# Performance work log

Hardware: AMD Instinct MI355X
Metric: run time of the kernel (lower is better)

The kernel has to match this reference:

```python
import jax, jax.numpy as jnp
import numpy as np

B, S, H = 8, 2048, 256

def setup_inputs() -> dict:
    key = jax.random.key(0)
    ks = jax.random.split(key, 7)
    sc = 0.05
    return {
        "inputs": jax.random.normal(ks[0], (B, S, H), dtype=jnp.float32),
        "Wq": jax.random.normal(ks[1], (H, H), dtype=jnp.float32) * sc,
        "bq": jax.random.normal(ks[2], (H,), dtype=jnp.float32) * sc,
        "Wk": jax.random.normal(ks[3], (H, H), dtype=jnp.float32) * sc,
        "bk": jax.random.normal(ks[4], (H,), dtype=jnp.float32) * sc,
        "Wv": jax.random.normal(ks[5], (H, H), dtype=jnp.float32) * sc,
        "bv": jax.random.normal(ks[6], (H,), dtype=jnp.float32) * sc,
    }

def reference(inputs, Wq, bq, Wk, bk, Wv, bv):
    # nn.Linear: y = x @ W.T + b
    q = jnp.einsum("bsh,oh->bso", inputs, Wq) + bq
    k = jnp.einsum("bsh,oh->bso", inputs, Wk) + bk
    v = jnp.einsum("bsh,oh->bso", inputs, Wv) + bv
    hidden = q.shape[-1]
    # NOTE: original scales by sqrt(hidden^2) == hidden (not sqrt(hidden))
    scores = jnp.einsum("bqh,bkh->bqk", q, k) / jnp.float32(hidden)
    # NOTE: original applies softmax over dim=1 (the query axis), not the last axis
    weights = jax.nn.softmax(scores, axis=1)
    return jnp.einsum("bqk,bkh->bqh", weights, v)
```

## Files before the change

### kernel.cpp

```cpp
#include <hip/hip_runtime.h>
#include <hip/hip_bf16.h>

#define B_ 8
#define S_ 2048
#define H_ 256
#define BS_ (B_*S_)

typedef __attribute__((ext_vector_type(8))) short bf16x8;
typedef __attribute__((ext_vector_type(4))) short bf16x4;
typedef __attribute__((ext_vector_type(4))) float f32x4;

static __device__ inline short f2bf(float f) {
  union { float f; unsigned int u; } a; a.f = f;
  unsigned int u = a.u;
  unsigned int r = (u + 0x7fffu + ((u >> 16) & 1u)) >> 16;
  return (short)r;
}

static __device__ inline float bf2f(short s) {
  union { float f; unsigned int u; } a;
  a.u = ((unsigned int)(unsigned short)s) << 16;
  return a.f;
}

static __device__ inline f32x4 mfma16(bf16x8 a, bf16x8 b, f32x4 c) {
  return __builtin_amdgcn_mfma_f32_16x16x32_bf16(a, b, c, 0, 0, 0);
}

static __device__ inline void gl_lds16(const short* g, short* l) {
  __builtin_amdgcn_global_load_lds(
      (const __attribute__((address_space(1))) void*)g,
      (__attribute__((address_space(3))) void*)l, 16, 0, 0);
}

#define NW4 (H_ * H_ / 4)
#define NWTOT (3 * NW4)
#define NALLW (NWTOT + BS_ / 4)

__global__ __launch_bounds__(256) void cvt_bf16(
    const float* __restrict__ Wq, const float* __restrict__ Wk,
    const float* __restrict__ Wv,
    short* __restrict__ wqb, short* __restrict__ wkb, short* __restrict__ wvb,
    float* __restrict__ den)
{
  int stride = gridDim.x * blockDim.x;
  for (int i = blockIdx.x * blockDim.x + threadIdx.x; i < NALLW; i += stride) {
    if (i >= NWTOT) {
      float4 z = {0.f, 0.f, 0.f, 0.f};
      *(float4*)(den + (size_t)(i - NWTOT) * 4) = z;
      continue;
    }
    int w = i >> 14;
    int off = i & (NW4 - 1);
    const float* src = (w == 0) ? Wq : (w == 1) ? Wk : Wv;
    short* dst = (w == 0) ? wqb : (w == 1) ? wkb : wvb;
    float4 v = *(const float4*)(src + off * 4);
    bf16x4 p;
    p[0] = f2bf(v.x); p[1] = f2bf(v.y); p[2] = f2bf(v.z); p[3] = f2bf(v.w);
    *(bf16x4*)(dst + off * 4) = p;
  }
}

__global__ __launch_bounds__(256) void qkv_proj(
    const float* __restrict__ x,
    const short* __restrict__ Wq, const float* __restrict__ bq,
    const short* __restrict__ Wk, const float* __restrict__ bk,
    const short* __restrict__ Wv, const float* __restrict__ bv,
    short* __restrict__ Qo, short* __restrict__ Ko, short* __restrict__ VTo)
{
  const int tid  = threadIdx.x;
  const int wave = tid >> 6;
  const int lane = tid & 63;
  const int quad = lane >> 4;
  const int l16  = lane & 15;
  const int y    = blockIdx.y;

  const short* W    = (y == 0) ? Wq : (y == 1) ? Wk : Wv;
  const float* bias = (y == 0) ? bq : (y == 1) ? bk : bv;
  const int sblk = blockIdx.x * 64;

  __shared__ short wbufA[16 * 512];
  __shared__ short xbufA[4 * 512];
  __shared__ short wbufB[16 * 512];
  __shared__ short xbufB[4 * 512];

  f32x4 zero = {0.f, 0.f, 0.f, 0.f};
  f32x4 acc[4][4];
#pragma unroll
  for (int i = 0; i < 4; i++)
#pragma unroll
    for (int j = 0; j < 4; j++) acc[i][j] = zero;

#define QKV_XLOAD(fa, fb, ch)                                             \
  {                                                                       \
    const float* xg = x + (size_t)(sblk + wave * 16 + l16) * H_ + (ch) * 32 + quad * 8; \
    fa = *(const float4*)xg;                                              \
    fb = *(const float4*)(xg + 4);                                        \
  }

#define QKV_XWRITE(xb_, fa, fb)                                           \
  {                                                                       \
    bf16x8 p;                                                             \
    p[0] = f2bf(fa.x); p[1] = f2bf(fa.y); p[2] = f2bf(fa.z); p[3] = f2bf(fa.w); \
    p[4] = f2bf(fb.x); p[5] = f2bf(fb.y); p[6] = f2bf(fb.z); p[7] = f2bf(fb.w); \
    *(bf16x8*)((xb_) + wave * 512 + lane * 8) = p;                        \
  }

#define QKV_STAGE_W(wb, ch)                                               \
  {                                                                       \
    _Pragma("unroll")                                                     \
    for (int i = 0; i < 4; i++) {                                         \
      int r = wave * 4 + i;                                               \
      gl_lds16(W + (r * 16 + l16) * H_ + (ch) * 32 + quad * 8, (wb) + r * 512); \
    }                                                                     \
  }

#define QKV_MFMA(wb, xb_)                                                 \
  {                                                                       \
    bf16x8 af[4];                                                         \
    _Pragma("unroll")                                                     \
    for (int st = 0; st < 4; st++)                                        \
      af[st] = *(const bf16x8*)((xb_) + st * 512 + lane * 8);             \
    _Pragma("unroll")                                                     \
    for (int i = 0; i < 4; i++) {                                         \
      bf16x8 bb = *(const bf16x8*)((wb) + (wave * 4 + i) * 512 + lane * 8); \
      _Pragma("unroll")                                                   \
      for (int st = 0; st < 4; st++)                                      \
        acc[st][i] = mfma16(af[st], bb, acc[st][i]);                      \
    }                                                                     \
  }

  float4 xa0, xb0, xa1, xb1;
  QKV_XLOAD(xa0, xb0, 0);
  QKV_STAGE_W(wbufA, 0);
  QKV_XWRITE(xbufA, xa0, xb0);
#pragma unroll
  for (int i2 = 0; i2 < 4; i2++) {
    __syncthreads();
    QKV_XLOAD(xa1, xb1, 2 * i2 + 1);
    QKV_STAGE_W(wbufB, 2 * i2 + 1);
    QKV_MFMA(wbufA, xbufA);
    QKV_XWRITE(xbufB, xa1, xb1);
    __syncthreads();
    if (i2 < 3) {
      QKV_XLOAD(xa0, xb0, 2 * i2 + 2);
      QKV_STAGE_W(wbufA, 2 * i2 + 2);
    }
    QKV_MFMA(wbufB, xbufB);
    if (i2 < 3) QKV_XWRITE(xbufA, xa0, xb0);
  }
#undef QKV_XLOAD
#undef QKV_XWRITE
#undef QKV_STAGE_W
#undef QKV_MFMA

  if (y < 2) {
    short* dst = (y == 0) ? Qo : Ko;
#pragma unroll
    for (int i = 0; i < 4; i++) {
      int col = (wave * 4 + i) * 16 + l16;
      float bvl = bias[col];
#pragma unroll
      for (int st = 0; st < 4; st++) {
#pragma unroll
        for (int r = 0; r < 4; r++) {
          int row = sblk + st * 16 + quad * 4 + r;
          dst[row * H_ + col] = f2bf(acc[st][i][r] + bvl);
        }
      }
    }
  } else {
#pragma unroll
    for (int i = 0; i < 4; i++) {
      int col = (wave * 4 + i) * 16 + l16;
      float bvl = bias[col];
#pragma unroll
      for (int st = 0; st < 4; st++) {
        int row0  = sblk + st * 16 + quad * 4;
        int b_idx = row0 >> 11;
        int k0    = row0 & (S_ - 1);
        bf16x4 pk;
#pragma unroll
        for (int r = 0; r < 4; r++) pk[r] = f2bf(acc[st][i][r] + bvl);
        *(bf16x4*)(VTo + (size_t)b_idx * H_ * S_ + (size_t)col * S_ + k0) = pk;
      }
    }
  }
}

__global__ __launch_bounds__(256, 2) void scores(
    const short* __restrict__ Q, const short* __restrict__ K,
    short* __restrict__ Pf, float* __restrict__ den)
{
  const int tid  = threadIdx.x;
  const int wave = tid >> 6;
  const int lane = tid & 63;
  const int quad = lane >> 4;
  const int l16  = lane & 15;
  const int ktg = blockIdx.x & 3;
  const int qt  = (blockIdx.x >> 2) & 15;
  const int b   = blockIdx.x >> 6;

  const short* Qb = Q + b * S_ * H_;
  const short* Kb = K + b * S_ * H_;
  const int qcol0 = qt * 128;

  __shared__ short qbuf[64 * 512];

  bf16x8 kreg[2][2][8];
  {
    const short* kb = Kb + ((ktg * 4) * 128 + wave * 32 + l16) * H_ + quad * 8;
#pragma unroll
    for (int kf = 0; kf < 2; kf++)
#pragma unroll
      for (int ch = 0; ch < 8; ch++)
        kreg[0][kf][ch] = *(const bf16x8*)(kb + kf * 16 * H_ + ch * 32);
  }

#pragma unroll
  for (int i = 0; i < 16; i++) {
    int region = wave * 16 + i;
    int qf = region >> 3;
    int ch = region & 7;
    gl_lds16(Qb + (qcol0 + qf * 16 + l16) * H_ + ch * 32 + quad * 8,
             qbuf + region * 512);
  }
  __syncthreads();

  const int quadA = quad >> 1;
  const int j0    = (quad & 1) * 4;

#pragma unroll
  for (int t = 0; t < 4; t++) {
    if (t < 3) {
      const short* kb = Kb + ((ktg * 4 + t + 1) * 128 + wave * 32 + l16) * H_ + quad * 8;
#pragma unroll
      for (int kf = 0; kf < 2; kf++)
#pragma unroll
        for (int ch = 0; ch < 8; ch++)
          kreg[(t + 1) & 1][kf][ch] = *(const bf16x8*)(kb + kf * 16 * H_ + ch * 32);
    }

    f32x4 zero = {0.f, 0.f, 0.f, 0.f};
    f32x4 acc[2][8];
#pragma unroll
    for (int i = 0; i < 2; i++)
#pragma unroll
      for (int j = 0; j < 8; j++) acc[i][j] = zero;

#pragma unroll
    for (int ch = 0; ch < 8; ch++) {
#pragma unroll
      for (int qf = 0; qf < 8; qf++) {
        bf16x8 bq = *(const bf16x8*)(qbuf + (qf * 8 + ch) * 512 + lane * 8);
        acc[0][qf] = mfma16(kreg[t & 1][0][ch], bq, acc[0][qf]);
        acc[1][qf] = mfma16(kreg[t & 1][1][ch], bq, acc[1][qf]);
      }
    }

    const int kt    = ktg * 4 + t;
    const int krow0 = kt * 128 + wave * 32;
    const int kw    = krow0 >> 5;

    float rs[2][4] = {{0.f,0.f,0.f,0.f},{0.f,0.f,0.f,0.f}};
#pragma unroll
    for (int kf = 0; kf < 2; kf++) {
#pragma unroll
      for (int qf = 0; qf < 8; qf++) {
        bf16x4 pk;
#pragma unroll
        for (int r = 0; r < 4; r++) {
          float e = __expf(acc[kf][qf][r] * (1.0f / H_));
          rs[kf][r] += e;
          pk[r] = f2bf(e);
        }
        size_t tile = ((size_t)(b * 128 + qt * 8 + qf) << 6) + kw;
        *(bf16x4*)(Pf + (tile << 9) + ((2 * kf + quadA) * 16 + l16) * 8 + j0) = pk;
      }
    }

#pragma unroll
    for (int kf = 0; kf < 2; kf++) {
#pragma unroll
      for (int r = 0; r < 4; r++) {
        float v = rs[kf][r];
        v += __shfl_xor(v, 1, 64);
        v += __shfl_xor(v, 2, 64);
        v += __shfl_xor(v, 4, 64);
        v += __shfl_xor(v, 8, 64);
        if (l16 == 0)
          atomicAdd(&den[b * S_ + krow0 + kf * 16 + quad * 4 + r], v);
      }
    }
  }
}

__global__ __launch_bounds__(256) void vscale(
    short* __restrict__ VT, const float* __restrict__ den)
{
  int i = blockIdx.x * 256 + threadIdx.x;
  int b  = i >> 17;
  int k0 = (i & 511) << 2;
  float4 df = *(const float4*)(den + b * S_ + k0);
  bf16x4 v = *(bf16x4*)(VT + (size_t)i * 4);
  bf16x4 o;
  o[0] = f2bf(bf2f(v[0]) / df.x);
  o[1] = f2bf(bf2f(v[1]) / df.y);
  o[2] = f2bf(bf2f(v[2]) / df.z);
  o[3] = f2bf(bf2f(v[3]) / df.w);
  *(bf16x4*)(VT + (size_t)i * 4) = o;
}

__global__ __launch_bounds__(256) void pv(
    const short* __restrict__ Pf, const short* __restrict__ VTs,
    float* __restrict__ out)
{
  const int tid  = threadIdx.x;
  const int wave = tid >> 6;
  const int lane = tid & 63;
  const int quad = lane >> 4;
  const int l16  = lane & 15;
  const int bx = blockIdx.x;
  const int qt = bx >> 4;
  const int b  = (bx >> 1) & 7;
  const int hs = bx & 1;

  __shared__ short vbufA[32 * 512];
  __shared__ short vbufB[32 * 512];

  const int qt16 = qt * 4 + wave;
  const short* VTb = VTs + (size_t)b * H_ * S_ + (size_t)(hs * 128) * S_;
  const size_t tilebase = ((size_t)(b * 128 + qt16) * 64) << 9;

  f32x4 zero = {0.f, 0.f, 0.f, 0.f};
  f32x4 acc[8];
#pragma unroll
  for (int i = 0; i < 8; i++) acc[i] = zero;

  bf16x8 pregA[4], pregB[4];

#define PV_STAGE_V(vb, kc)                                                  \
  {                                                                         \
    _Pragma("unroll")                                                       \
    for (int i = 0; i < 8; i++) {                                           \
      int id = wave * 8 + i;                                                \
      int n  = id >> 2;                                                     \
      int kw = id & 3;                                                      \
      const short* g = VTb + (size_t)(n * 16 + l16) * S_ + (kc) + kw * 32 + quad * 8; \
      gl_lds16(g, (vb) + id * 512);                                         \
    }                                                                       \
  }

#define PV_LOAD_P(pr, kc)                                                   \
  {                                                                         \
    _Pragma("unroll")                                                       \
    for (int kwi = 0; kwi < 4; kwi++)                                       \
      pr[kwi] = *(const bf16x8*)(Pf + tilebase + (size_t)(((kc) >> 5) + kwi) * 512 + lane * 8); \
  }

#define PV_MFMA(vb, pr)                                                     \
  {                                                                         \
    _Pragma("unroll")                                                       \
    for (int kw = 0; kw < 4; kw++) {                                        \
      _Pragma("unroll")                                                     \
      for (int n = 0; n < 8; n++) {                                         \
        bf16x8 vvb = *(const bf16x8*)((vb) + (n * 4 + kw) * 512 + lane * 8); \
        acc[n] = mfma16(pr[kw], vvb, acc[n]);                               \
      }                                                                     \
    }                                                                       \
  }

  PV_STAGE_V(vbufA, 0);
  PV_LOAD_P(pregA, 0);
#pragma unroll
  for (int i2 = 0; i2 < 8; i2++) {
    __syncthreads();
    PV_STAGE_V(vbufB, (2 * i2 + 1) * 128);
    PV_LOAD_P(pregB, (2 * i2 + 1) * 128);
    PV_MFMA(vbufA, pregA);
    __syncthreads();
    if (i2 < 7) {
      PV_STAGE_V(vbufA, (2 * i2 + 2) * 128);
      PV_LOAD_P(pregA, (2 * i2 + 2) * 128);
    }
    PV_MFMA(vbufB, pregB);
  }
#undef PV_STAGE_V
#undef PV_LOAD_P
#undef PV_MFMA

  const int q0 = qt16 * 16;
#pragma unroll
  for (int n = 0; n < 8; n++) {
    int col = hs * 128 + n * 16 + l16;
#pragma unroll
    for (int r = 0; r < 4; r++) {
      int q = q0 + quad * 4 + r;
      out[((size_t)b * S_ + q) * H_ + col] = acc[n][r];
    }
  }
}

extern "C" void kernel_launch(void* const* d_in, const int* in_sizes, int n_in,
                              void* d_out, int out_size, void* d_ws, size_t ws_size,
                              hipStream_t stream) {
  const float* x  = (const float*)d_in[0];
  const float* Wq = (const float*)d_in[1];
  const float* bq = (const float*)d_in[2];
  const float* Wk = (const float*)d_in[3];
  const float* bk = (const float*)d_in[4];
  const float* Wv = (const float*)d_in[5];
  const float* bv = (const float*)d_in[6];

  short* xb  = (short*)d_ws;
  short* wqb = xb  + (size_t)BS_ * H_;
  short* wkb = wqb + H_ * H_;
  short* wvb = wkb + H_ * H_;
  short* Qs  = wvb + H_ * H_;
  short* Ks  = Qs  + (size_t)BS_ * H_;
  short* VT  = Ks  + (size_t)BS_ * H_;
  short* P   = VT  + (size_t)BS_ * H_;
  float* den = (float*)(P + (size_t)B_ * S_ * S_);
  float* outp = (float*)d_out;

  cvt_bf16<<<208, 256, 0, stream>>>(Wq, Wk, Wv, wqb, wkb, wvb, den);
  qkv_proj<<<dim3(BS_ / 64, 3), 256, 0, stream>>>(x, wqb, bq, wkb, bk, wvb, bv, Qs, Ks, VT);
  scores<<<512, 256, 0, stream>>>(Qs, Ks, P, den);
  vscale<<<4096, 256, 0, stream>>>(VT, den);
  pv<<<512, 256, 0, stream>>>(P, VT, outp);
}
```

Baseline: 187.5 us.

## Recompute scores in fused PV kernel instead of materializing P matrix

The scores kernel now only accumulates the per-key softmax denominators and no longer writes the bf16 probability matrix. A fused PV kernel recomputes QK^T per 128-key chunk, applies exp and a reciprocal of the denominator, stages P in LDS and multiplies by V directly. This removes the large P write/read round trip through global memory and the separate vscale pass. The cost is doing the QK^T product twice, running a grid of 256 blocks at launch bounds of 1, and using single-buffered LDS with no prefetch of K or V.

```diff
diff --git a/kernel.cpp b/kernel.cpp
--- a/kernel.cpp
+++ b/kernel.cpp
@@ -188,9 +188,9 @@
   }
 }
 
-__global__ __launch_bounds__(256, 2) void scores(
+__global__ __launch_bounds__(256, 2) void scores_den(
     const short* __restrict__ Q, const short* __restrict__ K,
-    short* __restrict__ Pf, float* __restrict__ den)
+    float* __restrict__ den)
 {
   const int tid  = threadIdx.x;
   const int wave = tid >> 6;
@@ -227,9 +227,6 @@
   }
   __syncthreads();
 
-  const int quadA = quad >> 1;
-  const int j0    = (quad & 1) * 4;
-
 #pragma unroll
   for (int t = 0; t < 4; t++) {
     if (t < 3) {
@@ -258,24 +255,16 @@
       }
     }
 
-    const int kt    = ktg * 4 + t;
-    const int krow0 = kt * 128 + wave * 32;
-    const int kw    = krow0 >> 5;
+    const int krow0 = (ktg * 4 + t) * 128 + wave * 32;
 
     float rs[2][4] = {{0.f,0.f,0.f,0.f},{0.f,0.f,0.f,0.f}};
 #pragma unroll
     for (int kf = 0; kf < 2; kf++) {
 #pragma unroll
       for (int qf = 0; qf < 8; qf++) {
-        bf16x4 pk;
-#pragma unroll
-        for (int r = 0; r < 4; r++) {
-          float e = __expf(acc[kf][qf][r] * (1.0f / H_));
-          rs[kf][r] += e;
-          pk[r] = f2bf(e);
-        }
-        size_t tile = ((size_t)(b * 128 + qt * 8 + qf) << 6) + kw;
-        *(bf16x4*)(Pf + (tile << 9) + ((2 * kf + quadA) * 16 + l16) * 8 + j0) = pk;
+#pragma unroll
+        for (int r = 0; r < 4; r++)
+          rs[kf][r] += __expf(acc[kf][qf][r] * (1.0f / H_));
       }
     }
 
@@ -295,24 +284,9 @@
   }
 }
 
-__global__ __launch_bounds__(256) void vscale(
-    short* __restrict__ VT, const float* __restrict__ den)
-{
-  int i = blockIdx.x * 256 + threadIdx.x;
-  int b  = i >> 17;
-  int k0 = (i & 511) << 2;
-  float4 df = *(const float4*)(den + b * S_ + k0);
-  bf16x4 v = *(bf16x4*)(VT + (size_t)i * 4);
-  bf16x4 o;
-  o[0] = f2bf(bf2f(v[0]) / df.x);
-  o[1] = f2bf(bf2f(v[1]) / df.y);
-  o[2] = f2bf(bf2f(v[2]) / df.z);
-  o[3] = f2bf(bf2f(v[3]) / df.w);
-  *(bf16x4*)(VT + (size_t)i * 4) = o;
-}
-
-__global__ __launch_bounds__(256) void pv(
-    const short* __restrict__ Pf, const short* __restrict__ VTs,
+__global__ __launch_bounds__(256, 1) void pv_fused(
+    const short* __restrict__ Q, const short* __restrict__ K,
+    const short* __restrict__ VTs, const float* __restrict__ den,
     float* __restrict__ out)
 {
   const int tid  = threadIdx.x;
@@ -325,78 +299,127 @@
   const int b  = (bx >> 1) & 7;
   const int hs = bx & 1;
 
-  __shared__ short vbufA[32 * 512];
-  __shared__ short vbufB[32 * 512];
-
-  const int qt16 = qt * 4 + wave;
+  const short* Qb  = Q + b * S_ * H_;
+  const short* Kb  = K + b * S_ * H_;
   const short* VTb = VTs + (size_t)b * H_ * S_ + (size_t)(hs * 128) * S_;
-  const size_t tilebase = ((size_t)(b * 128 + qt16) * 64) << 9;
+  const float* denb = den + b * S_;
+  const int qcol0 = qt * 128;
+
+  __shared__ short qbuf[64 * 512];
+  __shared__ short pbuf[32 * 512];
+  __shared__ short vbuf[32 * 512];
 
   f32x4 zero = {0.f, 0.f, 0.f, 0.f};
-  f32x4 acc[8];
-#pragma unroll
-  for (int i = 0; i < 8; i++) acc[i] = zero;
-
-  bf16x8 pregA[4], pregB[4];
-
-#define PV_STAGE_V(vb, kc)                                                  \
-  {                                                                         \
-    _Pragma("unroll")                                                       \
-    for (int i = 0; i < 8; i++) {                                           \
-      int id = wave * 8 + i;                                                \
-      int n  = id >> 2;                                                     \
-      int kw = id & 3;                                                      \
-      const short* g = VTb + (size_t)(n * 16 + l16) * S_ + (kc) + kw * 32 + quad * 8; \
-      gl_lds16(g, (vb) + id * 512);                                         \
-    }                                                                       \
-  }
-
-#define PV_LOAD_P(pr, kc)                                                   \
-  {                                                                         \
-    _Pragma("unroll")                                                       \
-    for (int kwi = 0; kwi < 4; kwi++)                                       \
-      pr[kwi] = *(const bf16x8*)(Pf + tilebase + (size_t)(((kc) >> 5) + kwi) * 512 + lane * 8); \
-  }
-
-#define PV_MFMA(vb, pr)                                                     \
-  {                                                                         \
-    _Pragma("unroll")                                                       \
-    for (int kw = 0; kw < 4; kw++) {                                        \
-      _Pragma("unroll")                                                     \
-      for (int n = 0; n < 8; n++) {                                         \
-        bf16x8 vvb = *(const bf16x8*)((vb) + (n * 4 + kw) * 512 + lane * 8); \
-        acc[n] = mfma16(pr[kw], vvb, acc[n]);                               \
-      }                                                                     \
-    }                                                                       \
-  }
-
-  PV_STAGE_V(vbufA, 0);
-  PV_LOAD_P(pregA, 0);
-#pragma unroll
-  for (int i2 = 0; i2 < 8; i2++) {
+  f32x4 accpv[2][8];
+#pragma unroll
+  for (int i = 0; i < 2; i++)
+#pragma unroll
+    for (int j = 0; j < 8; j++) accpv[i][j] = zero;
+
+#pragma unroll
+  for (int i = 0; i < 16; i++) {
+    int region = wave * 16 + i;
+    int qf = region >> 3;
+    int ch = region & 7;
+    gl_lds16(Qb + (qcol0 + qf * 16 + l16) * H_ + ch * 32 + quad * 8,
+             qbuf + region * 512);
+  }
+  __syncthreads();
+
+  const int quadA = quad >> 1;
+  const int j0    = (quad & 1) * 4;
+
+  for (int t = 0; t < 16; t++) {
+    const int kc = t * 128;
+
+    bf16x8 kreg[2][8];
+    {
+      const short* kb = Kb + (kc + wave * 32 + l16) * H_ + quad * 8;
+#pragma unroll
+      for (int kf = 0; kf < 2; kf++)
+#pragma unroll
+        for (int ch = 0; ch < 8; ch++)
+          kreg[kf][ch] = *(const bf16x8*)(kb + kf * 16 * H_ + ch * 32);
+    }
+    float4 dv0 = *(const float4*)(denb + kc + wave * 32 + quad * 4);
+    float4 dv1 = *(const float4*)(denb + kc + wave * 32 + 16 + quad * 4);
+
+#pragma unroll
+    for (int i = 0; i < 8; i++) {
+      int id = wave * 8 + i;
+      int n  = id >> 2;
+      int kw = id & 3;
+      gl_lds16(VTb + (size_t)(n * 16 + l16) * S_ + kc + kw * 32 + quad * 8,
+               vbuf + id * 512);
+    }
+
+#pragma unroll
+    for (int kf = 0; kf < 2; kf++) {
+      f32x4 a8[8];
+#pragma unroll
+      for (int j = 0; j < 8; j++) a8[j] = zero;
+#pragma unroll
+      for (int ch = 0; ch < 8; ch++) {
+#pragma unroll
+        for (int qf = 0; qf < 8; qf++) {
+          bf16x8 bq = *(const bf16x8*)(qbuf + (qf * 8 + ch) * 512 + lane * 8);
+          a8[qf] = mfma16(kreg[kf][ch], bq, a8[qf]);
+        }
+      }
+      float rd[4];
+      {
+        float dd[4];
+        if (kf == 0) { dd[0]=dv0.x; dd[1]=dv0.y; dd[2]=dv0.z; dd[3]=dv0.w; }
+        else         { dd[0]=dv1.x; dd[1]=dv1.y; dd[2]=dv1.z; dd[3]=dv1.w; }
+#pragma unroll
+        for (int r = 0; r < 4; r++) {
+          float rc = __builtin_amdgcn_rcpf(dd[r]);
+          rc = rc * (2.0f - dd[r] * rc);
+          rd[r] = rc;
+        }
+      }
+#pragma unroll
+      for (int qf = 0; qf < 8; qf++) {
+        bf16x4 pk;
+#pragma unroll
+        for (int r = 0; r < 4; r++)
+          pk[r] = f2bf(__expf(a8[qf][r] * (1.0f / H_)) * rd[r]);
+        *(bf16x4*)(pbuf + (qf * 4 + wave) * 512 +
+                   ((2 * kf + quadA) * 16 + l16) * 8 + j0) = pk;
+      }
+    }
     __syncthreads();
-    PV_STAGE_V(vbufB, (2 * i2 + 1) * 128);
-    PV_LOAD_P(pregB, (2 * i2 + 1) * 128);
-    PV_MFMA(vbufA, pregA);
+
+#pragma unroll
+    for (int qsub = 0; qsub < 2; qsub++) {
+      const int qidx = wave * 2 + qsub;
+      bf16x8 preg[4];
+#pragma unroll
+      for (int ks = 0; ks < 4; ks++)
+        preg[ks] = *(const bf16x8*)(pbuf + (qidx * 4 + ks) * 512 + lane * 8);
+#pragma unroll
+      for (int ks = 0; ks < 4; ks++) {
+#pragma unroll
+        for (int n = 0; n < 8; n++) {
+          bf16x8 vvb = *(const bf16x8*)(vbuf + (n * 4 + ks) * 512 + lane * 8);
+          accpv[qsub][n] = mfma16(preg[ks], vvb, accpv[qsub][n]);
+        }
+      }
+    }
     __syncthreads();
-    if (i2 < 7) {
-      PV_STAGE_V(vbufA, (2 * i2 + 2) * 128);
-      PV_LOAD_P(pregA, (2 * i2 + 2) * 128);
-    }
-    PV_MFMA(vbufB, pregB);
-  }
-#undef PV_STAGE_V
-#undef PV_LOAD_P
-#undef PV_MFMA
-
-  const int q0 = qt16 * 16;
-#pragma unroll
-  for (int n = 0; n < 8; n++) {
-    int col = hs * 128 + n * 16 + l16;
-#pragma unroll
-    for (int r = 0; r < 4; r++) {
-      int q = q0 + quad * 4 + r;
-      out[((size_t)b * S_ + q) * H_ + col] = acc[n][r];
+  }
+
+#pragma unroll
+  for (int qsub = 0; qsub < 2; qsub++) {
+    const int q0 = qt * 128 + (wave * 2 + qsub) * 16;
+#pragma unroll
+    for (int n = 0; n < 8; n++) {
+      int col = hs * 128 + n * 16 + l16;
+#pragma unroll
+      for (int r = 0; r < 4; r++) {
+        int q = q0 + quad * 4 + r;
+        out[((size_t)b * S_ + q) * H_ + col] = accpv[qsub][n][r];
+      }
     }
   }
 }
@@ -425,7 +448,6 @@
 
   cvt_bf16<<<208, 256, 0, stream>>>(Wq, Wk, Wv, wqb, wkb, wvb, den);
   qkv_proj<<<dim3(BS_ / 64, 3), 256, 0, stream>>>(x, wqb, bq, wkb, bk, wvb, bv, Qs, Ks, VT);
-  scores<<<512, 256, 0, stream>>>(Qs, Ks, P, den);
-  vscale<<<4096, 256, 0, stream>>>(VT, den);
-  pv<<<512, 256, 0, stream>>>(P, VT, outp);
-}
+  scores_den<<<512, 256, 0, stream>>>(Qs, Ks, den);
+  pv_fused<<<256, 256, 0, stream>>>(Qs, Ks, VT, den, outp);
+}
```

New measurement: 236.0 us. +25.9%, slower.

## Recompute normalized scores inside PV kernel instead of materializing P

Applied to the files above, without the earlier changes.

The scores kernel now only accumulates column denominators. A new fused PV kernel recomputes Q·K^T per 128-key chunk, applies exp and reciprocal of the denominator, stages P in shared memory, and multiplies by V. This removes the large bf16 P write/read and the separate V scaling pass, at the cost of computing QK^T twice (once per head half as well) and a less overlapped pipeline with extra barriers.

```diff
diff --git a/kernel.cpp b/kernel.cpp
--- a/kernel.cpp
+++ b/kernel.cpp
@@ -188,9 +188,9 @@
   }
 }
 
-__global__ __launch_bounds__(256, 2) void scores(
+__global__ __launch_bounds__(256, 2) void scores_den(
     const short* __restrict__ Q, const short* __restrict__ K,
-    short* __restrict__ Pf, float* __restrict__ den)
+    float* __restrict__ den)
 {
   const int tid  = threadIdx.x;
   const int wave = tid >> 6;
@@ -227,9 +227,6 @@
   }
   __syncthreads();
 
-  const int quadA = quad >> 1;
-  const int j0    = (quad & 1) * 4;
-
 #pragma unroll
   for (int t = 0; t < 4; t++) {
     if (t < 3) {
@@ -258,24 +255,16 @@
       }
     }
 
-    const int kt    = ktg * 4 + t;
-    const int krow0 = kt * 128 + wave * 32;
-    const int kw    = krow0 >> 5;
+    const int krow0 = (ktg * 4 + t) * 128 + wave * 32;
 
     float rs[2][4] = {{0.f,0.f,0.f,0.f},{0.f,0.f,0.f,0.f}};
 #pragma unroll
     for (int kf = 0; kf < 2; kf++) {
 #pragma unroll
       for (int qf = 0; qf < 8; qf++) {
-        bf16x4 pk;
-#pragma unroll
-        for (int r = 0; r < 4; r++) {
-          float e = __expf(acc[kf][qf][r] * (1.0f / H_));
-          rs[kf][r] += e;
-          pk[r] = f2bf(e);
-        }
-        size_t tile = ((size_t)(b * 128 + qt * 8 + qf) << 6) + kw;
-        *(bf16x4*)(Pf + (tile << 9) + ((2 * kf + quadA) * 16 + l16) * 8 + j0) = pk;
+#pragma unroll
+        for (int r = 0; r < 4; r++)
+          rs[kf][r] += __expf(acc[kf][qf][r] * (1.0f / H_));
       }
     }
 
@@ -295,24 +284,9 @@
   }
 }
 
-__global__ __launch_bounds__(256) void vscale(
-    short* __restrict__ VT, const float* __restrict__ den)
-{
-  int i = blockIdx.x * 256 + threadIdx.x;
-  int b  = i >> 17;
-  int k0 = (i & 511) << 2;
-  float4 df = *(const float4*)(den + b * S_ + k0);
-  bf16x4 v = *(bf16x4*)(VT + (size_t)i * 4);
-  bf16x4 o;
-  o[0] = f2bf(bf2f(v[0]) / df.x);
-  o[1] = f2bf(bf2f(v[1]) / df.y);
-  o[2] = f2bf(bf2f(v[2]) / df.z);
-  o[3] = f2bf(bf2f(v[3]) / df.w);
-  *(bf16x4*)(VT + (size_t)i * 4) = o;
-}
-
-__global__ __launch_bounds__(256) void pv(
-    const short* __restrict__ Pf, const short* __restrict__ VTs,
+__global__ __launch_bounds__(256, 2) void pv_fused(
+    const short* __restrict__ Q, const short* __restrict__ K,
+    const short* __restrict__ VTs, const float* __restrict__ den,
     float* __restrict__ out)
 {
   const int tid  = threadIdx.x;
@@ -325,78 +299,133 @@
   const int b  = (bx >> 1) & 7;
   const int hs = bx & 1;
 
-  __shared__ short vbufA[32 * 512];
-  __shared__ short vbufB[32 * 512];
-
-  const int qt16 = qt * 4 + wave;
+  const short* Qb  = Q + b * S_ * H_;
+  const short* Kb  = K + b * S_ * H_;
   const short* VTb = VTs + (size_t)b * H_ * S_ + (size_t)(hs * 128) * S_;
-  const size_t tilebase = ((size_t)(b * 128 + qt16) * 64) << 9;
+  const float* denb = den + b * S_;
+  const int qcol0 = qt * 64;
+
+  __shared__ short qbuf[32 * 512];
+  __shared__ short pbuf[16 * 512];
+  __shared__ short vbuf[32 * 512];
 
   f32x4 zero = {0.f, 0.f, 0.f, 0.f};
-  f32x4 acc[8];
-#pragma unroll
-  for (int i = 0; i < 8; i++) acc[i] = zero;
-
-  bf16x8 pregA[4], pregB[4];
-
-#define PV_STAGE_V(vb, kc)                                                  \
+  f32x4 accpv[8];
+#pragma unroll
+  for (int i = 0; i < 8; i++) accpv[i] = zero;
+
+#pragma unroll
+  for (int i = 0; i < 8; i++) {
+    int region = wave * 8 + i;
+    int qf = region >> 3;
+    int ch = region & 7;
+    gl_lds16(Qb + (qcol0 + qf * 16 + l16) * H_ + ch * 32 + quad * 8,
+             qbuf + region * 512);
+  }
+
+  bf16x8 kregA[2][8], kregB[2][8];
+  float4 dvA0, dvA1, dvB0, dvB1;
+  {
+    const short* kb = Kb + (wave * 32 + l16) * H_ + quad * 8;
+#pragma unroll
+    for (int kf = 0; kf < 2; kf++)
+#pragma unroll
+      for (int ch = 0; ch < 8; ch++)
+        kregA[kf][ch] = *(const bf16x8*)(kb + kf * 16 * H_ + ch * 32);
+    dvA0 = *(const float4*)(denb + wave * 32 + quad * 4);
+    dvA1 = *(const float4*)(denb + wave * 32 + 16 + quad * 4);
+  }
+  __syncthreads();
+
+  const int quadA = quad >> 1;
+  const int j0    = (quad & 1) * 4;
+
+#define FCHUNK(kr, d0, d1, nkr, nd0, nd1, t, DOPF)                          \
   {                                                                         \
+    const int kc = (t) * 128;                                               \
     _Pragma("unroll")                                                       \
     for (int i = 0; i < 8; i++) {                                           \
       int id = wave * 8 + i;                                                \
       int n  = id >> 2;                                                     \
       int kw = id & 3;                                                      \
-      const short* g = VTb + (size_t)(n * 16 + l16) * S_ + (kc) + kw * 32 + quad * 8; \
-      gl_lds16(g, (vb) + id * 512);                                         \
+      gl_lds16(VTb + (size_t)(n * 16 + l16) * S_ + kc + kw * 32 + quad * 8, \
+               vbuf + id * 512);                                            \
     }                                                                       \
-  }
-
-#define PV_LOAD_P(pr, kc)                                                   \
-  {                                                                         \
     _Pragma("unroll")                                                       \
-    for (int kwi = 0; kwi < 4; kwi++)                                       \
-      pr[kwi] = *(const bf16x8*)(Pf + tilebase + (size_t)(((kc) >> 5) + kwi) * 512 + lane * 8); \
-  }
-
-#define PV_MFMA(vb, pr)                                                     \
-  {                                                                         \
+    for (int kf = 0; kf < 2; kf++) {                                        \
+      f32x4 a8[4];                                                          \
+      _Pragma("unroll")                                                     \
+      for (int j = 0; j < 4; j++) a8[j] = zero;                             \
+      _Pragma("unroll")                                                     \
+      for (int ch = 0; ch < 8; ch++) {                                      \
+        _Pragma("unroll")                                                   \
+        for (int qf = 0; qf < 4; qf++) {                                    \
+          bf16x8 bq = *(const bf16x8*)(qbuf + (qf * 8 + ch) * 512 + lane * 8); \
+          a8[qf] = mfma16(kr[kf][ch], bq, a8[qf]);                          \
+        }                                                                   \
+      }                                                                     \
+      float rd[4];                                                          \
+      {                                                                     \
+        float dd[4];                                                        \
+        if (kf == 0) { dd[0]=d0.x; dd[1]=d0.y; dd[2]=d0.z; dd[3]=d0.w; }    \
+        else         { dd[0]=d1.x; dd[1]=d1.y; dd[2]=d1.z; dd[3]=d1.w; }    \
+        _Pragma("unroll")                                                   \
+        for (int r = 0; r < 4; r++) {                                       \
+          float rc = __builtin_amdgcn_rcpf(dd[r]);                          \
+          rc = rc * (2.0f - dd[r] * rc);                                    \
+          rd[r] = rc;                                                       \
+        }                                                                   \
+      }                                                                     \
+      _Pragma("unroll")                                                     \
+      for (int qf = 0; qf < 4; qf++) {                                      \
+        bf16x4 pk;                                                          \
+        _Pragma("unroll")                                                   \
+        for (int r = 0; r < 4; r++)                                         \
+          pk[r] = f2bf(__expf(a8[qf][r] * (1.0f / H_)) * rd[r]);            \
+        *(bf16x4*)(pbuf + (qf * 4 + wave) * 512 +                           \
+                   ((2 * kf + quadA) * 16 + l16) * 8 + j0) = pk;            \
+      }                                                                     \
+    }                                                                       \
+    if (DOPF) {                                                             \
+      const short* kb = Kb + ((t + 1) * 128 + wave * 32 + l16) * H_ + quad * 8; \
+      _Pragma("unroll")                                                     \
+      for (int kf = 0; kf < 2; kf++)                                        \
+        _Pragma("unroll")                                                   \
+        for (int ch = 0; ch < 8; ch++)                                      \
+          nkr[kf][ch] = *(const bf16x8*)(kb + kf * 16 * H_ + ch * 32);      \
+      nd0 = *(const float4*)(denb + (t + 1) * 128 + wave * 32 + quad * 4);  \
+      nd1 = *(const float4*)(denb + (t + 1) * 128 + wave * 32 + 16 + quad * 4); \
+    }                                                                       \
+    __syncthreads();                    \
+    bf16x8 preg[4];                                                         \
     _Pragma("unroll")                                                       \
-    for (int kw = 0; kw < 4; kw++) {                                        \
+    for (int ks = 0; ks < 4; ks++)                                          \
+      preg[ks] = *(const bf16x8*)(pbuf + (wave * 4 + ks) * 512 + lane * 8); \
+    _Pragma("unroll")                                                       \
+    for (int ks = 0; ks < 4; ks++) {                                        \
       _Pragma("unroll")                                                     \
       for (int n = 0; n < 8; n++) {                                         \
-        bf16x8 vvb = *(const bf16x8*)((vb) + (n * 4 + kw) * 512 + lane * 8); \
-        acc[n] = mfma16(pr[kw], vvb, acc[n]);                               \
+        bf16x8 vvb = *(const bf16x8*)(vbuf + (n * 4 + ks) * 512 + lane * 8); \
+        accpv[n] = mfma16(preg[ks], vvb, accpv[n]);                         \
       }                                                                     \
     }                                                                       \
-  }
-
-  PV_STAGE_V(vbufA, 0);
-  PV_LOAD_P(pregA, 0);
-#pragma unroll
+    __syncthreads();           \
+  }
+
   for (int i2 = 0; i2 < 8; i2++) {
-    __syncthreads();
-    PV_STAGE_V(vbufB, (2 * i2 + 1) * 128);
-    PV_LOAD_P(pregB, (2 * i2 + 1) * 128);
-    PV_MFMA(vbufA, pregA);
-    __syncthreads();
-    if (i2 < 7) {
-      PV_STAGE_V(vbufA, (2 * i2 + 2) * 128);
-      PV_LOAD_P(pregA, (2 * i2 + 2) * 128);
-    }
-    PV_MFMA(vbufB, pregB);
-  }
-#undef PV_STAGE_V
-#undef PV_LOAD_P
-#undef PV_MFMA
-
-  const int q0 = qt16 * 16;
+    FCHUNK(kregA, dvA0, dvA1, kregB, dvB0, dvB1, 2 * i2, 1);
+    FCHUNK(kregB, dvB0, dvB1, kregA, dvA0, dvA1, 2 * i2 + 1, (i2 < 7));
+  }
+#undef FCHUNK
+
+  const int q0 = qt * 64 + wave * 16;
 #pragma unroll
   for (int n = 0; n < 8; n++) {
     int col = hs * 128 + n * 16 + l16;
 #pragma unroll
     for (int r = 0; r < 4; r++) {
       int q = q0 + quad * 4 + r;
-      out[((size_t)b * S_ + q) * H_ + col] = acc[n][r];
+      out[((size_t)b * S_ + q) * H_ + col] = accpv[n][r];
     }
   }
 }
@@ -425,7 +454,6 @@
 
   cvt_bf16<<<208, 256, 0, stream>>>(Wq, Wk, Wv, wqb, wkb, wvb, den);
   qkv_proj<<<dim3(BS_ / 64, 3), 256, 0, stream>>>(x, wqb, bq, wkb, bk, wvb, bv, Qs, Ks, VT);
-  scores<<<512, 256, 0, stream>>>(Qs, Ks, P, den);
-  vscale<<<4096, 256, 0, stream>>>(VT, den);
-  pv<<<512, 256, 0, stream>>>(P, VT, outp);
-}
+  scores_den<<<512, 256, 0, stream>>>(Qs, Ks, den);
+  pv_fused<<<512, 256, 0, stream>>>(Qs, Ks, VT, den, outp);
+}
```

Result: slower. 235.4 us (+25.6%).
